# Kernel tuning notes

Hardware: AMD Instinct MI355X
Metric: run time of the kernel (lower is better)

The kernel has to match this reference:

```python
import jax, jax.numpy as jnp
import numpy as np

B, E, IMG, PATCH, C, HEADS, DEPTH = 128, 512, 256, 32, 384, 3, 6
GRID = IMG // PATCH            # 8
NPATCH = GRID * GRID           # 64
N = NPATCH + 1                 # 65 tokens incl cls
HD = C // HEADS                # 128
MLP_H = 4 * C                  # 1536
SCALE = HD ** -0.5


def setup_inputs() -> dict:
    key = jax.random.key(0)
    ks = jax.random.split(key, 12)
    s = 0.02
    return {
        "images": jax.random.normal(ks[0], (B, 3, IMG, IMG), jnp.float32),
        "patch_w": jax.random.normal(ks[1], (C, 3, PATCH, PATCH), jnp.float32) * s,
        "patch_b": jnp.zeros((C,), jnp.float32),
        "cls_token": jax.random.normal(ks[2], (1, 1, C), jnp.float32) * s,
        "pos_embed": jax.random.normal(ks[3], (1, N, C), jnp.float32) * s,
        "norm1_w": jnp.ones((DEPTH, C), jnp.float32),
        "norm1_b": jnp.zeros((DEPTH, C), jnp.float32),
        "qkv_w": jax.random.normal(ks[4], (DEPTH, 3 * C, C), jnp.float32) * s,
        "proj_w": jax.random.normal(ks[5], (DEPTH, C, C), jnp.float32) * s,
        "proj_b": jnp.zeros((DEPTH, C), jnp.float32),
        "norm2_w": jnp.ones((DEPTH, C), jnp.float32),
        "norm2_b": jnp.zeros((DEPTH, C), jnp.float32),
        "fc1_w": jax.random.normal(ks[6], (DEPTH, MLP_H, C), jnp.float32) * s,
        "fc1_b": jnp.zeros((DEPTH, MLP_H), jnp.float32),
        "fc2_w": jax.random.normal(ks[7], (DEPTH, C, MLP_H), jnp.float32) * s,
        "fc2_b": jnp.zeros((DEPTH, C), jnp.float32),
        "norm_w": jnp.ones((C,), jnp.float32),
        "norm_b": jnp.zeros((C,), jnp.float32),
        "edge_index": jax.random.randint(ks[8], (2, E), 0, B, dtype=jnp.int32),
    }


def _ln(x, w, b):
    mu = x.mean(-1, keepdims=True)
    v = ((x - mu) ** 2).mean(-1, keepdims=True)
    return (x - mu) * jax.lax.rsqrt(v + 1e-5) * w + b


def _forward(images, patch_w, patch_b, cls_token, pos_embed,
             norm1_w, norm1_b, qkv_w, proj_w, proj_b,
             norm2_w, norm2_b, fc1_w, fc1_b, fc2_w, fc2_b,
             norm_w, norm_b, edge_index):
    src, dst = edge_index[0], edge_index[1]  # PyG: x_j = x[src], aggregate over dst
    cnt = jax.ops.segment_sum(jnp.ones((E,), jnp.float32), dst, num_segments=B)
    cnt = jnp.clip(cnt, 1.0)[:, None, None]  # scatter-mean denominator

    # PatchEmbed: conv stride = kernel = PATCH
    p = jax.lax.conv_general_dilated(images, patch_w, (PATCH, PATCH), 'VALID',
                                     dimension_numbers=('NCHW', 'OIHW', 'NCHW'))
    p = p + patch_b[None, :, None, None]
    p = p.reshape(B, C, NPATCH).transpose(0, 2, 1)          # [B, 64, C]
    x = jnp.concatenate([jnp.broadcast_to(cls_token, (B, 1, C)), p], axis=1) + pos_embed  # [B, N, C]

    for d in range(DEPTH):
        # MEConv2: LN -> qkv -> per-edge attention (q,v from target i; k from source j) -> proj -> scatter-mean
        y = _ln(x, norm1_w[d], norm1_b[d])
        qkv = (y @ qkv_w[d].T).reshape(B, N, 3, HEADS, HD)
        q = qkv[:, :, 0][dst]   # [E, N, H, HD]
        k = qkv[:, :, 1][src]
        v = qkv[:, :, 2][dst]
        attn = jnp.einsum('enhd,emhd->ehnm', q, k) * SCALE   # [E, H, N, N]
        a = jax.nn.softmax(attn, axis=-1)
        o = jnp.einsum('ehnm,emhd->enhd', a, v).reshape(E, N, C)
        msg = o @ proj_w[d].T + proj_b[d]                    # [E, N, C]
        agg = jax.ops.segment_sum(msg, dst, num_segments=B) / cnt
        x = x + agg
        # Block MLP residual
        h = _ln(x, norm2_w[d], norm2_b[d])
        h = jax.nn.gelu(h @ fc1_w[d].T + fc1_b[d], approximate=False)
        x = x + (h @ fc2_w[d].T + fc2_b[d])

    x = _ln(x, norm_w, norm_b)
    return x[:, 0]  # cls token features, [B, C]


def reference(images, patch_w, patch_b, cls_token, pos_embed,
              norm1_w, norm1_b, qkv_w, proj_w, proj_b,
              norm2_w, norm2_b, fc1_w, fc1_b, fc2_w, fc2_b,
              norm_w, norm_b, edge_index):
    return _forward(images, patch_w, patch_b, cls_token, pos_embed,
                    norm1_w, norm1_b, qkv_w, proj_w, proj_b,
                    norm2_w, norm2_b, fc1_w, fc1_b, fc2_w, fc2_b,
                    norm_w, norm_b, edge_index)
```

## Files before the change

### kernel.cpp

```cpp
#include <hip/hip_runtime.h>

typedef unsigned short u16;
typedef unsigned int   u32;
typedef __attribute__((ext_vector_type(4))) float f32x4;
using bf16x8 = __attribute__((ext_vector_type(8))) __bf16;

#define AS1 __attribute__((address_space(1)))
#define AS3 __attribute__((address_space(3)))

#define SCALE_ 0.08838834764831845f

#define X_OFF      0ull
#define Y_OFF      12779520ull
#define QKV_OFF    19169280ull
#define OBAR_OFF   38338560ull
#define SCR_OFF    44728320ull
#define PE_OFF     70287360ull
#define WB_OFF     95059968ull
#define ELIST_OFF  118652928ull
#define EOFF_OFF   118654976ull
#define INV_OFF    118655744ull
#define BSC_OFF    118656256ull
#define DLIST_OFF  118656768ull

#define PW_E   0
#define QW_E   1179648
#define PRW_E  3833856
#define F1W_E  4718592
#define F2W_E  8257536

#define R0_ 294912
#define R1_ 958464
#define R2_ 1179648
#define R3_ 2064384
#define R4_ 2949120

#define PVS 104

__device__ __forceinline__ u16 f2bf(float f){
  union { float fv; u32 u; } x; x.fv = f;
  u32 r = x.u + 0x7FFFu + ((x.u >> 16) & 1u);
  return (u16)(r >> 16);
}
__device__ __forceinline__ float bf2f(u16 u){
  union { u32 u; float fv; } x; x.u = ((u32)u) << 16;
  return x.fv;
}
__device__ __forceinline__ void gld16(const void* g, void* l){
  __builtin_amdgcn_global_load_lds((AS1 void*)g, (AS3 void*)l, 16, 0, 0);
}

__global__ void cvt_all_k(const float* __restrict__ s0, const float* __restrict__ s1,
                          const float* __restrict__ s2, const float* __restrict__ s3,
                          const float* __restrict__ s4, u16* __restrict__ d){
  int i = blockIdx.x*256 + threadIdx.x;
  const float* s; int rel;
  if (i < R0_)      { s = s0; rel = i; }
  else if (i < R1_) { s = s1; rel = i - R0_; }
  else if (i < R2_) { s = s2; rel = i - R1_; }
  else if (i < R3_) { s = s3; rel = i - R2_; }
  else              { s = s4; rel = i - R3_; }
  float4 v = ((const float4*)s)[rel];
  ushort4 o; o.x=f2bf(v.x); o.y=f2bf(v.y); o.z=f2bf(v.z); o.w=f2bf(v.w);
  ((ushort4*)d)[i] = o;
}

__global__ void im2col_k(const float* __restrict__ img, u16* __restrict__ A){
  int idx = blockIdx.x*256 + threadIdx.x;
  int m = idx / 384, k8 = idx - m*384;
  int k = k8 * 8;
  int c  = k >> 10;
  int kh = (k >> 5) & 31;
  int kw = k & 31;
  int b = m >> 6, p = m & 63;
  int ph = p >> 3, pw = p & 7;
  const float* src = img + ((size_t)(b*3 + c)*256 + ph*32 + kh)*256 + pw*32 + kw;
  float4 v0 = *(const float4*)src;
  float4 v1 = *(const float4*)(src + 4);
  uint4 ov; u16* tp = (u16*)&ov;
  tp[0]=f2bf(v0.x); tp[1]=f2bf(v0.y); tp[2]=f2bf(v0.z); tp[3]=f2bf(v0.w);
  tp[4]=f2bf(v1.x); tp[5]=f2bf(v1.y); tp[6]=f2bf(v1.z); tp[7]=f2bf(v1.w);
  *(uint4*)(A + (size_t)m*3072 + k) = ov;
}

__global__ void cls_init_k(const float* __restrict__ cls, const float* __restrict__ pos,
                           float* __restrict__ X){
  int idx = blockIdx.x*256 + threadIdx.x;
  int b = idx / 384, c = idx - b*384;
  X[(size_t)b*65*384 + c] = cls[c] + pos[c];
}

__global__ __launch_bounds__(128) void edge_prep_k(const int* __restrict__ ei,
                                                   int* __restrict__ elist,
                                                   int* __restrict__ eoff,
                                                   float* __restrict__ inv,
                                                   float* __restrict__ bsc,
                                                   int* __restrict__ dlist){
  __shared__ int srcS[512];
  __shared__ int dstS[512];
  __shared__ int cnt[128];
  const int t = threadIdx.x;
  for (int e = t; e < 512; e += 128){ srcS[e] = ei[e]; dstS[e] = ei[512 + e]; }
  __syncthreads();
  int c = 0;
  for (int e = 0; e < 512; e++) c += (dstS[e] == t) ? 1 : 0;
  cnt[t] = c;
  __syncthreads();
  int off = 0;
  for (int b = 0; b < t; b++) off += cnt[b];
  eoff[t] = off;
  if (t == 127) eoff[128] = off + c;
  inv[t] = 1.0f / (float)(c > 1 ? c : 1);
  bsc[t] = (c > 0) ? 1.0f : 0.0f;
  int p = off;
  for (int e = 0; e < 512; e++){
    if (dstS[e] == t){ elist[p] = srcS[e]; dlist[p] = t; p++; }
  }
}

__global__ __launch_bounds__(256) void ln_k(const float* __restrict__ X,
                                            const float* __restrict__ w,
                                            const float* __restrict__ b,
                                            u16* __restrict__ Y){
  int row  = blockIdx.x*4 + (threadIdx.x >> 6);
  int lane = threadIdx.x & 63;
  const float* xr = X + (size_t)row*384;
  float v[6]; float s = 0.f;
  #pragma unroll
  for (int i=0;i<6;i++){ v[i] = xr[lane + i*64]; s += v[i]; }
  #pragma unroll
  for (int m=1;m<64;m<<=1) s += __shfl_xor(s, m);
  float mu = s * (1.f/384.f);
  float q = 0.f;
  #pragma unroll
  for (int i=0;i<6;i++){ float d = v[i]-mu; q += d*d; }
  #pragma unroll
  for (int m=1;m<64;m<<=1) q += __shfl_xor(q, m);
  float rs = rsqrtf(q*(1.f/384.f) + 1e-5f);
  u16* yr = Y + (size_t)row*384;
  #pragma unroll
  for (int i=0;i<6;i++){ int e = lane + i*64; yr[e] = f2bf((v[i]-mu)*rs*w[e] + b[e]); }
}

__global__ __launch_bounds__(256) void ln_final_k(const float* __restrict__ X,
                                                  const float* __restrict__ w,
                                                  const float* __restrict__ b,
                                                  float* __restrict__ out){
  int bb   = blockIdx.x*4 + (threadIdx.x >> 6);
  int lane = threadIdx.x & 63;
  const float* xr = X + (size_t)bb*65*384;
  float v[6]; float s = 0.f;
  #pragma unroll
  for (int i=0;i<6;i++){ v[i] = xr[lane + i*64]; s += v[i]; }
  #pragma unroll
  for (int m=1;m<64;m<<=1) s += __shfl_xor(s, m);
  float mu = s * (1.f/384.f);
  float q = 0.f;
  #pragma unroll
  for (int i=0;i<6;i++){ float d = v[i]-mu; q += d*d; }
  #pragma unroll
  for (int m=1;m<64;m<<=1) q += __shfl_xor(q, m);
  float rs = rsqrtf(q*(1.f/384.f) + 1e-5f);
  #pragma unroll
  for (int i=0;i<6;i++){ int e = lane + i*64; out[(size_t)bb*384 + e] = (v[i]-mu)*rs*w[e] + b[e]; }
}

template<int MODE>
__global__ __launch_bounds__(256) void gemm_nt(
    const u16* __restrict__ A, const u16* __restrict__ W, int K,
    u16* __restrict__ outb, float* __restrict__ outf,
    const float* __restrict__ bias, const float* __restrict__ extra, int ldout)
{
  __shared__ u16 As[2][4096];
  __shared__ u16 Bs[2][8192];
  const int t    = threadIdx.x;
  const int lane = t & 63;
  const int w    = t >> 6;
  const int wr   = w >> 1, wc = w & 1;
  const int m0 = blockIdx.x * 64, n0 = blockIdx.y * 128;
  const int rs = t >> 3;
  const int cs = (((t & 7) ^ (rs & 7))) * 8;
  const u16* Ag = A + (size_t)(m0 + rs) * K + cs;
  const u16* Wg = W + (size_t)(n0 + rs) * K + cs;
  const size_t K32 = (size_t)K * 32;
  const int ln15 = lane & 15, l8 = (lane >> 4) * 8, lq = (lane >> 4) << 2;
  const int swz = (ln15 & 7) << 3;

  f32x4 acc[2][4] = {};
  const int nk = K >> 6;
  int cur = 0;

  gld16(Ag,           &As[0][t*8]);
  gld16(Ag + K32,     &As[0][2048 + t*8]);
  gld16(Wg,           &Bs[0][t*8]);
  gld16(Wg + K32,     &Bs[0][2048 + t*8]);
  gld16(Wg + 2*K32,   &Bs[0][4096 + t*8]);
  gld16(Wg + 3*K32,   &Bs[0][6144 + t*8]);
  __syncthreads();

  for (int kt = 1; kt <= nk; kt++){
    if (kt < nk){
      const int k0 = kt << 6;
      const int nb = cur ^ 1;
      gld16(Ag + k0,         &As[nb][t*8]);
      gld16(Ag + K32 + k0,   &As[nb][2048 + t*8]);
      gld16(Wg + k0,         &Bs[nb][t*8]);
      gld16(Wg + K32 + k0,   &Bs[nb][2048 + t*8]);
      gld16(Wg + 2*K32 + k0, &Bs[nb][4096 + t*8]);
      gld16(Wg + 3*K32 + k0, &Bs[nb][6144 + t*8]);
    }
    #pragma unroll
    for (int ks = 0; ks < 2; ks++){
      const int col = (ks*32 + l8) ^ swz;
      bf16x8 af[2], bfr[4];
      #pragma unroll
      for (int mi=0; mi<2; mi++)
        af[mi] = *(const bf16x8*)(&As[cur][(wr*32 + mi*16 + ln15)*64 + col]);
      #pragma unroll
      for (int ni=0; ni<4; ni++)
        bfr[ni] = *(const bf16x8*)(&Bs[cur][(wc*64 + ni*16 + ln15)*64 + col]);
      #pragma unroll
      for (int mi=0; mi<2; mi++)
        #pragma unroll
        for (int ni=0; ni<4; ni++)
          acc[mi][ni] = __builtin_amdgcn_mfma_f32_16x16x32_bf16(af[mi], bfr[ni], acc[mi][ni], 0,0,0);
    }
    if (kt < nk) __syncthreads();
    cur ^= 1;
  }

  #pragma unroll
  for (int mi=0; mi<2; mi++){
    #pragma unroll
    for (int j=0; j<4; j++){
      const int m = m0 + wr*32 + mi*16 + lq + j;
      #pragma unroll
      for (int ni=0; ni<4; ni++){
        const int n = n0 + wc*64 + ni*16 + ln15;
        float v = acc[mi][ni][j];
        if constexpr (MODE == 0){
          outb[(size_t)m*ldout + n] = f2bf(v);
        } else if constexpr (MODE == 1){
          int bb = m >> 6, p = m & 63;
          outf[((size_t)bb*65 + 1 + p)*384 + n] = v + bias[n] + extra[(1+p)*384 + n];
        } else if constexpr (MODE == 2){
          outf[(size_t)m*384 + n] += v + extra[m/65]*bias[n];
        } else if constexpr (MODE == 3){
          float g = v + bias[n];
          g = 0.5f*g*(1.f + erff(g*0.70710678118f));
          outb[(size_t)m*ldout + n] = f2bf(g);
        } else {
          outf[(size_t)m*384 + n] += v + bias[n];
        }
      }
    }
  }
}

__global__ __launch_bounds__(320) void qk_k(
    const u16* __restrict__ qkv, u16* __restrict__ Pe,
    const int* __restrict__ elist, const int* __restrict__ dlist)
{
  __shared__ u16 Qs[80*128];
  __shared__ u16 Ks[80*128];
  const int ee = blockIdx.x, h = blockIdx.y;
  const int t = threadIdx.x, w = t >> 6, lane = t & 63;
  const int ln15 = lane & 15, lq = (lane >> 4) << 2, l8 = (lane >> 4) * 8;
  const int b = dlist[ee], s = elist[ee];
  const size_t qbase = (size_t)b*65*1152 + h*128;
  const size_t kbase = (size_t)s*65*1152 + 384 + h*128;

  for (int idx = t; idx < 1040; idx += 320){
    int n = idx >> 4, g = idx & 15;
    int cc = (g ^ (n & 15)) * 8;
    gld16(qkv + qbase + (size_t)n*1152 + cc, Qs + idx*8);
    gld16(qkv + kbase + (size_t)n*1152 + cc, Ks + idx*8);
  }
  __syncthreads();

  const int swz = ln15 << 3;
  u16* pe = Pe + ((size_t)ee*3 + h)*6400;
  {
    const int rt = w;
    f32x4 sc[5] = {};
    #pragma unroll
    for (int ks=0; ks<4; ks++){
      const int col = (ks*32 + l8) ^ swz;
      bf16x8 a = *(const bf16x8*)(Qs + (rt*16 + ln15)*128 + col);
      #pragma unroll
      for (int ct=0; ct<5; ct++){
        bf16x8 kb = *(const bf16x8*)(Ks + (ct*16 + ln15)*128 + col);
        sc[ct] = __builtin_amdgcn_mfma_f32_16x16x32_bf16(a, kb, sc[ct], 0,0,0);
      }
    }
    #pragma unroll
    for (int j=0;j<4;j++){
      const int r = rt*16 + lq + j;
      const bool c4ok = (ln15 == 0);
      float ev[5];
      float mx = -1e30f;
      #pragma unroll
      for (int ct=0; ct<5; ct++){
        float sv = sc[ct][j] * SCALE_;
        ev[ct] = sv;
        if (ct < 4 || c4ok) mx = fmaxf(mx, sv);
      }
      #pragma unroll
      for (int mm=1; mm<16; mm<<=1) mx = fmaxf(mx, __shfl_xor(mx, mm));
      float se = 0.f;
      #pragma unroll
      for (int ct=0; ct<5; ct++){
        ev[ct] = (ct < 4 || c4ok) ? expf(ev[ct]-mx) : 0.f;
        se += ev[ct];
      }
      #pragma unroll
      for (int mm=1; mm<16; mm<<=1) se += __shfl_xor(se, mm);
      const float pscale = 1.f / se;
      if (r < 65){
        #pragma unroll
        for (int ct=0; ct<5; ct++)
          pe[r*80 + ct*16 + ln15] = f2bf(ev[ct]*pscale);
      }
    }
  }
}

__global__ __launch_bounds__(256) void pv_k(
    const u16* __restrict__ qkv, const u16* __restrict__ Pe,
    u16* __restrict__ obar, const int* __restrict__ eoff,
    const float* __restrict__ invc)
{
  __shared__ u16 Pb[80*PVS];
  __shared__ u16 Vt[128*PVS];
  const int b = blockIdx.x, h = blockIdx.y;
  const int t = threadIdx.x, w = t >> 6, lane = t & 63;
  const int ln15 = lane & 15, lq = (lane >> 4) << 2, l8 = (lane >> 4) * 8;
  const int e0 = eoff[b], e1 = eoff[b+1];
  const float inv = invc[b];

  float acc[25];
  #pragma unroll
  for (int i=0;i<25;i++) acc[i] = 0.f;
  for (int ee = e0; ee < e1; ee++){
    const u16* pe = Pe + ((size_t)ee*3 + h)*6400;
    #pragma unroll
    for (int i=0;i<25;i++) acc[i] += bf2f(pe[t + i*256]);
  }
  #pragma unroll
  for (int i=0;i<25;i++){
    int idx = t + i*256; int r = idx/80, c = idx - r*80;
    Pb[r*PVS + c] = f2bf(acc[i]*inv);
  }
  for (int idx = t; idx < 80*16; idx += 256)
    Pb[(idx>>4)*PVS + 80 + (idx & 15)] = 0;
  for (int idx = t; idx < 128*31; idx += 256){
    int d = idx / 31, m = 65 + (idx - d*31);
    Vt[d*PVS + m] = 0;
  }
  const size_t vbase = (size_t)b*65*1152 + 768 + h*128;
  for (int idx = t; idx < 1040; idx += 256){
    int m = idx >> 4, dc = (idx & 15)*8;
    uint4 v = *(const uint4*)(qkv + vbase + (size_t)m*1152 + dc);
    const u16* p = (const u16*)&v;
    #pragma unroll
    for (int i=0;i<8;i++) Vt[(dc+i)*PVS + m] = p[i];
  }
  __syncthreads();

  for (int ntile = w*2; ntile < w*2+2; ntile++){
    #pragma unroll
    for (int mt=0; mt<5; mt++){
      f32x4 oc = {};
      #pragma unroll
      for (int ks=0; ks<3; ks++){
        bf16x8 a  = *(const bf16x8*)(Pb + (mt*16 + ln15)*PVS + ks*32 + l8);
        bf16x8 vb = *(const bf16x8*)(Vt + (ntile*16 + ln15)*PVS + ks*32 + l8);
        oc = __builtin_amdgcn_mfma_f32_16x16x32_bf16(a, vb, oc, 0,0,0);
      }
      #pragma unroll
      for (int j=0;j<4;j++){
        int n = mt*16 + lq + j;
        if (n < 65) obar[((size_t)b*65 + n)*384 + h*128 + ntile*16 + ln15] = f2bf(oc[j]);
      }
    }
  }
}

extern "C" void kernel_launch(void* const* d_in, const int* in_sizes, int n_in,
                              void* d_out, int out_size, void* d_ws, size_t ws_size,
                              hipStream_t stream) {
  (void)in_sizes; (void)n_in; (void)out_size; (void)ws_size;
  const float* images  = (const float*)d_in[0];
  const float* patch_w = (const float*)d_in[1];
  const float* patch_b = (const float*)d_in[2];
  const float* cls_tok = (const float*)d_in[3];
  const float* pos_emb = (const float*)d_in[4];
  const float* n1w = (const float*)d_in[5];
  const float* n1b = (const float*)d_in[6];
  const float* qkvw = (const float*)d_in[7];
  const float* projw = (const float*)d_in[8];
  const float* projb = (const float*)d_in[9];
  const float* n2w = (const float*)d_in[10];
  const float* n2b = (const float*)d_in[11];
  const float* f1w = (const float*)d_in[12];
  const float* f1b = (const float*)d_in[13];
  const float* f2w = (const float*)d_in[14];
  const float* f2b = (const float*)d_in[15];
  const float* nw  = (const float*)d_in[16];
  const float* nb  = (const float*)d_in[17];
  const int*   eidx = (const int*)d_in[18];

  char* ws = (char*)d_ws;
  float* X   = (float*)(ws + X_OFF);
  u16*   Y   = (u16*)(ws + Y_OFF);
  u16*   QKV = (u16*)(ws + QKV_OFF);
  u16*   OB  = (u16*)(ws + OBAR_OFF);
  u16*   SCR = (u16*)(ws + SCR_OFF);
  u16*   PE  = (u16*)(ws + PE_OFF);
  u16*   WB  = (u16*)(ws + WB_OFF);
  int*   ELIST = (int*)(ws + ELIST_OFF);
  int*   EOFF  = (int*)(ws + EOFF_OFF);
  float* INV   = (float*)(ws + INV_OFF);
  float* BSC   = (float*)(ws + BSC_OFF);
  int*   DLIST = (int*)(ws + DLIST_OFF);

  cvt_all_k<<<11520, 256, 0, stream>>>(patch_w, qkvw, projw, f1w, f2w, WB);

  edge_prep_k<<<1, 128, 0, stream>>>(eidx, ELIST, EOFF, INV, BSC, DLIST);
  im2col_k<<<12288, 256, 0, stream>>>(images, SCR);
  cls_init_k<<<192, 256, 0, stream>>>(cls_tok, pos_emb, X);

  gemm_nt<1><<<dim3(128, 3), 256, 0, stream>>>(SCR, WB + PW_E, 3072,
                                               nullptr, X, patch_b, pos_emb, 0);

  for (int d = 0; d < 6; d++){
    ln_k<<<2080, 256, 0, stream>>>(X, n1w + d*384, n1b + d*384, Y);
    gemm_nt<0><<<dim3(130, 9), 256, 0, stream>>>(Y, WB + QW_E + (size_t)d*1152*384, 384,
                                                 QKV, nullptr, nullptr, nullptr, 1152);
    qk_k<<<dim3(512, 3), 320, 0, stream>>>(QKV, PE, ELIST, DLIST);
    pv_k<<<dim3(128, 3), 256, 0, stream>>>(QKV, PE, OB, EOFF, INV);
    gemm_nt<2><<<dim3(130, 3), 256, 0, stream>>>(OB, WB + PRW_E + (size_t)d*384*384, 384,
                                                 nullptr, X, projb + d*384, BSC, 0);
    ln_k<<<2080, 256, 0, stream>>>(X, n2w + d*384, n2b + d*384, Y);
    gemm_nt<3><<<dim3(130, 12), 256, 0, stream>>>(Y, WB + F1W_E + (size_t)d*1536*384, 384,
                                                  SCR, nullptr, f1b + d*1536, nullptr, 1536);
    gemm_nt<4><<<dim3(130, 3), 256, 0, stream>>>(SCR, WB + F2W_E + (size_t)d*384*1536, 1536,
                                                 nullptr, X, f2b + d*384, nullptr, 0);
  }

  ln_final_k<<<32, 256, 0, stream>>>(X, nw, nb, (float*)d_out);
}
```

Baseline: 874.0 us.

## Triple-buffer GEMM shared-memory tiles with explicit vmcnt waits

Replaces the double-buffered K loop in gemm_nt with a three-stage ring of LDS buffers. Global-to-LDS loads run two tiles ahead, and explicit s_waitcnt vmcnt counts wait only for the tile about to be consumed. The aim is to hide more global-load latency behind the MFMA work. The cost is 50% more LDS per block (72KB), which can lower occupancy, plus an extra barrier per iteration. Correctness depends on gld16 issuing exactly one vector-memory op per call.

```diff
diff --git a/kernel.cpp b/kernel.cpp
--- a/kernel.cpp
+++ b/kernel.cpp
@@ -171,8 +171,8 @@
     u16* __restrict__ outb, float* __restrict__ outf,
     const float* __restrict__ bias, const float* __restrict__ extra, int ldout)
 {
-  __shared__ u16 As[2][4096];
-  __shared__ u16 Bs[2][8192];
+  __shared__ u16 As[3][4096];
+  __shared__ u16 Bs[3][8192];
   const int t    = threadIdx.x;
   const int lane = t & 63;
   const int w    = t >> 6;
@@ -188,45 +188,52 @@
 
   f32x4 acc[2][4] = {};
   const int nk = K >> 6;
-  int cur = 0;
-
-  gld16(Ag,           &As[0][t*8]);
-  gld16(Ag + K32,     &As[0][2048 + t*8]);
-  gld16(Wg,           &Bs[0][t*8]);
-  gld16(Wg + K32,     &Bs[0][2048 + t*8]);
-  gld16(Wg + 2*K32,   &Bs[0][4096 + t*8]);
-  gld16(Wg + 3*K32,   &Bs[0][6144 + t*8]);
-  __syncthreads();
-
-  for (int kt = 1; kt <= nk; kt++){
-    if (kt < nk){
-      const int k0 = kt << 6;
-      const int nb = cur ^ 1;
-      gld16(Ag + k0,         &As[nb][t*8]);
-      gld16(Ag + K32 + k0,   &As[nb][2048 + t*8]);
-      gld16(Wg + k0,         &Bs[nb][t*8]);
-      gld16(Wg + K32 + k0,   &Bs[nb][2048 + t*8]);
-      gld16(Wg + 2*K32 + k0, &Bs[nb][4096 + t*8]);
-      gld16(Wg + 3*K32 + k0, &Bs[nb][6144 + t*8]);
-    }
+
+  auto STAGE = [&](int bb, int kt){
+    const int k0 = kt << 6;
+    gld16(Ag + k0,         &As[bb][t*8]);
+    gld16(Ag + K32 + k0,   &As[bb][2048 + t*8]);
+    gld16(Wg + k0,         &Bs[bb][t*8]);
+    gld16(Wg + K32 + k0,   &Bs[bb][2048 + t*8]);
+    gld16(Wg + 2*K32 + k0, &Bs[bb][4096 + t*8]);
+    gld16(Wg + 3*K32 + k0, &Bs[bb][6144 + t*8]);
+  };
+
+  STAGE(0, 0);
+  STAGE(1, 1);
+  int cb = 0, sb = 2;
+
+  for (int kt = 0; kt < nk; kt++){
+    if (kt + 2 < nk){
+      STAGE(sb, kt + 2);
+      asm volatile("s_waitcnt vmcnt(12)" ::: "memory");
+    } else if (kt + 2 == nk){
+      asm volatile("s_waitcnt vmcnt(6)" ::: "memory");
+    } else {
+      asm volatile("s_waitcnt vmcnt(0)" ::: "memory");
+    }
+    __builtin_amdgcn_s_barrier();
+    __builtin_amdgcn_sched_barrier(0);
     #pragma unroll
     for (int ks = 0; ks < 2; ks++){
       const int col = (ks*32 + l8) ^ swz;
       bf16x8 af[2], bfr[4];
       #pragma unroll
       for (int mi=0; mi<2; mi++)
-        af[mi] = *(const bf16x8*)(&As[cur][(wr*32 + mi*16 + ln15)*64 + col]);
+        af[mi] = *(const bf16x8*)(&As[cb][(wr*32 + mi*16 + ln15)*64 + col]);
       #pragma unroll
       for (int ni=0; ni<4; ni++)
-        bfr[ni] = *(const bf16x8*)(&Bs[cur][(wc*64 + ni*16 + ln15)*64 + col]);
+        bfr[ni] = *(const bf16x8*)(&Bs[cb][(wc*64 + ni*16 + ln15)*64 + col]);
       #pragma unroll
       for (int mi=0; mi<2; mi++)
         #pragma unroll
         for (int ni=0; ni<4; ni++)
           acc[mi][ni] = __builtin_amdgcn_mfma_f32_16x16x32_bf16(af[mi], bfr[ni], acc[mi][ni], 0,0,0);
     }
-    if (kt < nk) __syncthreads();
-    cur ^= 1;
+    __builtin_amdgcn_s_barrier();
+    __builtin_amdgcn_sched_barrier(0);
+    cb = (cb == 2) ? 0 : cb + 1;
+    sb = (sb == 2) ? 0 : sb + 1;
   }
 
   #pragma unroll
```

Result: no change. 889.3 us (+1.8%).

## Fuse LayerNorm into QKV and FC1 GEMM A-tile loading

Applied to the files above, without the earlier changes.

Removes the standalone LayerNorm kernels. The QKV and FC1 GEMMs now read fp32 X directly, normalize each 64-row tile in registers and write the bf16 result into a swizzled shared-memory A buffer that holds the full K=384. The weight tiles are double-buffered from global memory. This drops two launches per layer and the write/read round trip of the normalized bf16 activations, but each N-tile block recomputes the LayerNorm for its rows (9x and 12x redundancy) and uses about 80KB of LDS, which limits occupancy.

```diff
diff --git a/kernel.cpp b/kernel.cpp
--- a/kernel.cpp
+++ b/kernel.cpp
@@ -118,30 +118,6 @@
   }
 }
 
-__global__ __launch_bounds__(256) void ln_k(const float* __restrict__ X,
-                                            const float* __restrict__ w,
-                                            const float* __restrict__ b,
-                                            u16* __restrict__ Y){
-  int row  = blockIdx.x*4 + (threadIdx.x >> 6);
-  int lane = threadIdx.x & 63;
-  const float* xr = X + (size_t)row*384;
-  float v[6]; float s = 0.f;
-  #pragma unroll
-  for (int i=0;i<6;i++){ v[i] = xr[lane + i*64]; s += v[i]; }
-  #pragma unroll
-  for (int m=1;m<64;m<<=1) s += __shfl_xor(s, m);
-  float mu = s * (1.f/384.f);
-  float q = 0.f;
-  #pragma unroll
-  for (int i=0;i<6;i++){ float d = v[i]-mu; q += d*d; }
-  #pragma unroll
-  for (int m=1;m<64;m<<=1) q += __shfl_xor(q, m);
-  float rs = rsqrtf(q*(1.f/384.f) + 1e-5f);
-  u16* yr = Y + (size_t)row*384;
-  #pragma unroll
-  for (int i=0;i<6;i++){ int e = lane + i*64; yr[e] = f2bf((v[i]-mu)*rs*w[e] + b[e]); }
-}
-
 __global__ __launch_bounds__(256) void ln_final_k(const float* __restrict__ X,
                                                   const float* __restrict__ w,
                                                   const float* __restrict__ b,
@@ -238,19 +214,109 @@
       for (int ni=0; ni<4; ni++){
         const int n = n0 + wc*64 + ni*16 + ln15;
         float v = acc[mi][ni][j];
-        if constexpr (MODE == 0){
-          outb[(size_t)m*ldout + n] = f2bf(v);
-        } else if constexpr (MODE == 1){
+        if constexpr (MODE == 1){
           int bb = m >> 6, p = m & 63;
           outf[((size_t)bb*65 + 1 + p)*384 + n] = v + bias[n] + extra[(1+p)*384 + n];
         } else if constexpr (MODE == 2){
           outf[(size_t)m*384 + n] += v + extra[m/65]*bias[n];
-        } else if constexpr (MODE == 3){
+        } else {
+          outf[(size_t)m*384 + n] += v + bias[n];
+        }
+      }
+    }
+  }
+}
+
+template<int MODE>
+__global__ __launch_bounds__(256) void gemm_lnA(
+    const float* __restrict__ X, const float* __restrict__ lnw, const float* __restrict__ lnb,
+    const u16* __restrict__ W, u16* __restrict__ outb,
+    const float* __restrict__ bias, int ldout)
+{
+  __shared__ u16 Ash[64*384];
+  __shared__ u16 Bs[2][8192];
+  const int t = threadIdx.x, lane = t & 63, w = t >> 6;
+  const int wr = w >> 1, wc = w & 1;
+  const int m0 = blockIdx.x * 64, n0 = blockIdx.y * 128;
+  const int rsb = t >> 3;
+  const int csb = (((t & 7) ^ (rsb & 7))) * 8;
+  const u16* Wg = W + (size_t)(n0 + rsb) * 384 + csb;
+  const size_t K32 = 384ull * 32;
+  const int ln15 = lane & 15, l8 = (lane >> 4) * 8, lq = (lane >> 4) << 2;
+  const int swz = (ln15 & 7) << 3;
+
+  auto STAGE_B = [&](int bb, int kt){
+    const int k0 = kt << 6;
+    gld16(Wg + k0,         &Bs[bb][t*8]);
+    gld16(Wg + K32 + k0,   &Bs[bb][2048 + t*8]);
+    gld16(Wg + 2*K32 + k0, &Bs[bb][4096 + t*8]);
+    gld16(Wg + 3*K32 + k0, &Bs[bb][6144 + t*8]);
+  };
+  STAGE_B(0, 0);
+  STAGE_B(1, 1);
+
+  for (int i = 0; i < 16; i++){
+    const int r = w*16 + i;
+    const float* xr = X + (size_t)(m0 + r)*384;
+    float v[6]; float s = 0.f;
+    #pragma unroll
+    for (int j=0;j<6;j++){ v[j] = xr[lane + j*64]; s += v[j]; }
+    #pragma unroll
+    for (int mm=1;mm<64;mm<<=1) s += __shfl_xor(s, mm);
+    float mu = s * (1.f/384.f);
+    float q = 0.f;
+    #pragma unroll
+    for (int j=0;j<6;j++){ float d = v[j]-mu; q += d*d; }
+    #pragma unroll
+    for (int mm=1;mm<64;mm<<=1) q += __shfl_xor(q, mm);
+    float rsq = rsqrtf(q*(1.f/384.f) + 1e-5f);
+    #pragma unroll
+    for (int j=0;j<6;j++){
+      int e = lane + j*64;
+      int g = (e >> 3) ^ (r & 7);
+      Ash[r*384 + g*8 + (e & 7)] = f2bf((v[j]-mu)*rsq*lnw[e] + lnb[e]);
+    }
+  }
+  __syncthreads();
+
+  f32x4 acc[2][4] = {};
+  for (int kt = 0; kt < 6; kt++){
+    if (kt >= 1 && kt + 1 < 6) STAGE_B((kt+1) & 1, kt+1);
+    #pragma unroll
+    for (int ks = 0; ks < 2; ks++){
+      const int bcol = (ks*32 + l8) ^ swz;
+      const int agrp = (kt*8 + ks*4 + (l8 >> 3)) ^ (ln15 & 7);
+      bf16x8 af[2], bfr[4];
+      #pragma unroll
+      for (int mi=0; mi<2; mi++)
+        af[mi] = *(const bf16x8*)(&Ash[(wr*32 + mi*16 + ln15)*384 + agrp*8]);
+      #pragma unroll
+      for (int ni=0; ni<4; ni++)
+        bfr[ni] = *(const bf16x8*)(&Bs[kt & 1][(wc*64 + ni*16 + ln15)*64 + bcol]);
+      #pragma unroll
+      for (int mi=0; mi<2; mi++)
+        #pragma unroll
+        for (int ni=0; ni<4; ni++)
+          acc[mi][ni] = __builtin_amdgcn_mfma_f32_16x16x32_bf16(af[mi], bfr[ni], acc[mi][ni], 0,0,0);
+    }
+    if (kt + 1 < 6) __syncthreads();
+  }
+
+  #pragma unroll
+  for (int mi=0; mi<2; mi++){
+    #pragma unroll
+    for (int j=0; j<4; j++){
+      const int m = m0 + wr*32 + mi*16 + lq + j;
+      #pragma unroll
+      for (int ni=0; ni<4; ni++){
+        const int n = n0 + wc*64 + ni*16 + ln15;
+        float v = acc[mi][ni][j];
+        if constexpr (MODE == 0){
+          outb[(size_t)m*ldout + n] = f2bf(v);
+        } else {
           float g = v + bias[n];
           g = 0.5f*g*(1.f + erff(g*0.70710678118f));
           outb[(size_t)m*ldout + n] = f2bf(g);
-        } else {
-          outf[(size_t)m*384 + n] += v + bias[n];
         }
       }
     }
@@ -412,7 +478,6 @@
 
   char* ws = (char*)d_ws;
   float* X   = (float*)(ws + X_OFF);
-  u16*   Y   = (u16*)(ws + Y_OFF);
   u16*   QKV = (u16*)(ws + QKV_OFF);
   u16*   OB  = (u16*)(ws + OBAR_OFF);
   u16*   SCR = (u16*)(ws + SCR_OFF);
@@ -434,16 +499,16 @@
                                                nullptr, X, patch_b, pos_emb, 0);
 
   for (int d = 0; d < 6; d++){
-    ln_k<<<2080, 256, 0, stream>>>(X, n1w + d*384, n1b + d*384, Y);
-    gemm_nt<0><<<dim3(130, 9), 256, 0, stream>>>(Y, WB + QW_E + (size_t)d*1152*384, 384,
-                                                 QKV, nullptr, nullptr, nullptr, 1152);
+    gemm_lnA<0><<<dim3(130, 9), 256, 0, stream>>>(X, n1w + d*384, n1b + d*384,
+                                                  WB + QW_E + (size_t)d*1152*384,
+                                                  QKV, nullptr, 1152);
     qk_k<<<dim3(512, 3), 320, 0, stream>>>(QKV, PE, ELIST, DLIST);
     pv_k<<<dim3(128, 3), 256, 0, stream>>>(QKV, PE, OB, EOFF, INV);
     gemm_nt<2><<<dim3(130, 3), 256, 0, stream>>>(OB, WB + PRW_E + (size_t)d*384*384, 384,
                                                  nullptr, X, projb + d*384, BSC, 0);
-    ln_k<<<2080, 256, 0, stream>>>(X, n2w + d*384, n2b + d*384, Y);
-    gemm_nt<3><<<dim3(130, 12), 256, 0, stream>>>(Y, WB + F1W_E + (size_t)d*1536*384, 384,
-                                                  SCR, nullptr, f1b + d*1536, nullptr, 1536);
+    gemm_lnA<1><<<dim3(130, 12), 256, 0, stream>>>(X, n2w + d*384, n2b + d*384,
+                                                   WB + F1W_E + (size_t)d*1536*384,
+                                                   SCR, f1b + d*1536, 1536);
     gemm_nt<4><<<dim3(130, 3), 256, 0, stream>>>(SCR, WB + F2W_E + (size_t)d*384*1536, 1536,
                                                  nullptr, X, f2b + d*384, nullptr, 0);
   }
```

New measurement: 1.321 ms. +51.1%, slower.

## Halve GEMM K-tile to 32 with MFMA-fragment-ordered LDS layout for higher occupancy

Applied to the files above, without the earlier changes.

The bf16 NT GEMM now stages K in slices of 32 instead of 64, halving LDS per block. Tiles are written into LDS already in the per-lane MFMA fragment order, so each wave reads contiguous 16-byte chunks without the XOR swizzle. The launch bound now requests 6 blocks per CU, which caps registers per thread. The cost is twice as many K iterations and barriers, with less work between each sync to hide global load latency.

```diff
diff --git a/kernel.cpp b/kernel.cpp
--- a/kernel.cpp
+++ b/kernel.cpp
@@ -166,67 +166,56 @@
 }
 
 template<int MODE>
-__global__ __launch_bounds__(256) void gemm_nt(
+__global__ __launch_bounds__(256, 6) void gemm_nt(
     const u16* __restrict__ A, const u16* __restrict__ W, int K,
     u16* __restrict__ outb, float* __restrict__ outf,
     const float* __restrict__ bias, const float* __restrict__ extra, int ldout)
 {
-  __shared__ u16 As[2][4096];
-  __shared__ u16 Bs[2][8192];
+  __shared__ u16 As[2][2048];
+  __shared__ u16 Bs[2][4096];
   const int t    = threadIdx.x;
   const int lane = t & 63;
   const int w    = t >> 6;
   const int wr   = w >> 1, wc = w & 1;
   const int m0 = blockIdx.x * 64, n0 = blockIdx.y * 128;
-  const int rs = t >> 3;
-  const int cs = (((t & 7) ^ (rs & 7))) * 8;
-  const u16* Ag = A + (size_t)(m0 + rs) * K + cs;
-  const u16* Wg = W + (size_t)(n0 + rs) * K + cs;
-  const size_t K32 = (size_t)K * 32;
-  const int ln15 = lane & 15, l8 = (lane >> 4) * 8, lq = (lane >> 4) << 2;
-  const int swz = (ln15 & 7) << 3;
+  const int l63  = t & 63;
+  const int srow = (l63 & 15), sslot = l63 >> 4;
+  const int a_row = (t >> 6)*16 + srow;
+  const int b_row0 = (t >> 6)*16 + srow;
+  const int b_row1 = (4 + (t >> 6))*16 + srow;
+  const u16* Ag  = A + (size_t)(m0 + a_row) * K + sslot*8;
+  const u16* Wg0 = W + (size_t)(n0 + b_row0) * K + sslot*8;
+  const u16* Wg1 = W + (size_t)(n0 + b_row1) * K + sslot*8;
+  const int ln15 = lane & 15, lq = (lane >> 4) << 2;
 
   f32x4 acc[2][4] = {};
-  const int nk = K >> 6;
-  int cur = 0;
-
-  gld16(Ag,           &As[0][t*8]);
-  gld16(Ag + K32,     &As[0][2048 + t*8]);
-  gld16(Wg,           &Bs[0][t*8]);
-  gld16(Wg + K32,     &Bs[0][2048 + t*8]);
-  gld16(Wg + 2*K32,   &Bs[0][4096 + t*8]);
-  gld16(Wg + 3*K32,   &Bs[0][6144 + t*8]);
+  const int nk = K >> 5;
+
+  auto STAGE = [&](int bb, int k0){
+    gld16(Ag  + k0, &As[bb][t*8]);
+    gld16(Wg0 + k0, &Bs[bb][t*8]);
+    gld16(Wg1 + k0, &Bs[bb][2048 + t*8]);
+  };
+
+  STAGE(0, 0);
   __syncthreads();
 
   for (int kt = 1; kt <= nk; kt++){
-    if (kt < nk){
-      const int k0 = kt << 6;
-      const int nb = cur ^ 1;
-      gld16(Ag + k0,         &As[nb][t*8]);
-      gld16(Ag + K32 + k0,   &As[nb][2048 + t*8]);
-      gld16(Wg + k0,         &Bs[nb][t*8]);
-      gld16(Wg + K32 + k0,   &Bs[nb][2048 + t*8]);
-      gld16(Wg + 2*K32 + k0, &Bs[nb][4096 + t*8]);
-      gld16(Wg + 3*K32 + k0, &Bs[nb][6144 + t*8]);
-    }
-    #pragma unroll
-    for (int ks = 0; ks < 2; ks++){
-      const int col = (ks*32 + l8) ^ swz;
-      bf16x8 af[2], bfr[4];
-      #pragma unroll
-      for (int mi=0; mi<2; mi++)
-        af[mi] = *(const bf16x8*)(&As[cur][(wr*32 + mi*16 + ln15)*64 + col]);
+    if (kt < nk) STAGE(kt & 1, kt << 5);
+    const int cur = (kt - 1) & 1;
+    bf16x8 af[2], bfr[4];
+    #pragma unroll
+    for (int mi=0; mi<2; mi++)
+      af[mi] = *(const bf16x8*)(&As[cur][((wr*2 + mi)*64 + lane)*8]);
+    #pragma unroll
+    for (int ni=0; ni<4; ni++)
+      bfr[ni] = *(const bf16x8*)(&Bs[cur][((wc*4 + ni)*64 + lane)*8]);
+    #pragma unroll
+    for (int mi=0; mi<2; mi++)
       #pragma unroll
       for (int ni=0; ni<4; ni++)
-        bfr[ni] = *(const bf16x8*)(&Bs[cur][(wc*64 + ni*16 + ln15)*64 + col]);
-      #pragma unroll
-      for (int mi=0; mi<2; mi++)
-        #pragma unroll
-        for (int ni=0; ni<4; ni++)
-          acc[mi][ni] = __builtin_amdgcn_mfma_f32_16x16x32_bf16(af[mi], bfr[ni], acc[mi][ni], 0,0,0);
-    }
+        acc[mi][ni] = __builtin_amdgcn_mfma_f32_16x16x32_bf16(af[mi], bfr[ni], acc[mi][ni], 0,0,0);
     if (kt < nk) __syncthreads();
-    cur ^= 1;
   }
 
   #pragma unroll
```

Result: slower. 1.106 ms (+26.5%).
